# Kernel tuning notes

Hardware: AMD Instinct MI355X
Metric: run time of the kernel (lower is better)

The kernel has to match this reference:

```python
import jax, jax.numpy as jnp
import numpy as np

F_CTX = 16          # ctx_future_context_size
CONV_STRENGTH = 0.5 # ctx_conv_strength
LN_EPS = 1e-5


def _layernorm(x, w, eps=LN_EPS):
    mu = jnp.mean(x, axis=-1, keepdims=True)
    var = jnp.var(x, axis=-1, keepdims=True)
    return (x - mu) / jnp.sqrt(var + eps) * w


def setup_inputs() -> dict:
    key = jax.random.key(0)
    B, S, D, V = 2, 512, 1024, 32000
    k0, k1, k2, k3 = jax.random.split(key, 4)
    emb_norm = jax.random.normal(k0, (B, S, D), jnp.float32)
    W_lm = jax.random.normal(k1, (V, D), jnp.float32) * 0.02
    W_ctx = jax.random.normal(k2, (V, D), jnp.float32) * 0.02
    ln_w = jnp.ones((D,), jnp.float32)
    # labels cover seq_len + F - 1 future tokens (required by the gather/view)
    y = jax.random.randint(k3, (B, S + F_CTX - 1), 0, V, dtype=jnp.int32)
    return {"emb_norm": emb_norm, "W_lm": W_lm, "W_ctx": W_ctx, "ln_w": ln_w, "y": y}


def reference(emb_norm, W_lm, W_ctx, ln_w, y):
    B, S, D = emb_norm.shape
    V = W_lm.shape[0]
    F = F_CTX

    logits = jnp.einsum('bsd,vd->bsv', emb_norm, W_lm)             # lm_head.output_proj
    c = jnp.einsum('bsd,vd->bsv', _layernorm(emb_norm, ln_w), W_ctx)  # context_head

    # y_context[b, s, v] = count of v among the F future tokens y[b, s:s+F]
    # (faithful to gather(indices) + one_hot(...).sum(-2), without the huge one-hot)
    win = jnp.arange(S)[:, None] + jnp.arange(F)[None, :]          # (S, F)
    y_win = y[:, win]                                              # (B, S, F)
    b_idx = jnp.arange(B)[:, None, None]
    s_idx = jnp.arange(S)[None, :, None]
    y_context = jnp.zeros((B, S, V), jnp.float32).at[b_idx, s_idx, y_win].add(1.0)

    # weighted BCE-with-logits (mean over all elements, per-element weight)
    w = 1.0 + 0.5 * jnp.any(y_context > 1.0, axis=0).astype(jnp.float32)   # (S, V)
    t = (y_context > 0.0).astype(jnp.float32)
    bce = jnp.maximum(c, 0.0) - c * t + jnp.log1p(jnp.exp(-jnp.abs(c)))
    context_loss = jnp.mean(w * bce)

    # causal exponential-decay window sum over the last F positions of c
    ed = jnp.exp(-CONV_STRENGTH * jnp.arange(F - 1, -1, -1, dtype=jnp.float32))
    ed = ed / ed.sum()
    c_pad = jnp.pad(c, ((0, 0), (F - 1, 0), (0, 0)))
    context = jnp.zeros_like(c)
    for j in range(F):  # fixed small window (16)
        context = context + ed[j] * c_pad[:, j:j + S, :]

    logits = logits + context

    # cross entropy vs y[:, :-F+1] == y[:, :S], ignore_index = -1
    tgt = y[:, :S]
    logp = jax.nn.log_softmax(logits, axis=-1)
    valid = (tgt >= 0)
    tgt_safe = jnp.where(valid, tgt, 0)
    nll = -jnp.take_along_axis(logp, tgt_safe[..., None].astype(jnp.int32), axis=-1)[..., 0]
    loss = jnp.sum(nll * valid.astype(nll.dtype)) / jnp.maximum(jnp.sum(valid.astype(jnp.float32)), 1.0)

    return logits, loss, context_loss
```

## Files before the change

kernel.cpp:

```cpp
#include <hip/hip_runtime.h>
#include <hip/hip_bf16.h>

typedef unsigned short u16;
typedef unsigned int u32;
typedef __bf16 bf16x8 __attribute__((ext_vector_type(8)));
typedef float f32x4 __attribute__((ext_vector_type(4)));

#define SDIM 512
#define BDIM 2
#define DDIM 1024
#define VDIM 32000
#define FCTX 16
#define NROWS (BDIM * SDIM)
#define YSTR (SDIM + FCTX - 1)
#define CONV_CHUNK 64

__device__ __forceinline__ u16 f2bf(float f) {
    u32 u = __float_as_uint(f);
    u += 0x7fffu + ((u >> 16) & 1u);
    return (u16)(u >> 16);
}

__device__ __forceinline__ void gload_lds16(const void* g, void* l) {
    __builtin_amdgcn_global_load_lds((const __attribute__((address_space(1))) void*)g,
                                     (__attribute__((address_space(3))) void*)l, 16, 0, 0);
}

__global__ __launch_bounds__(256) void prep_a_kernel(
    const float* __restrict__ emb, const float* __restrict__ lnw,
    u16* __restrict__ Alm, u16* __restrict__ Actx)
{
    int row = blockIdx.x;
    int t = threadIdx.x;
    const float4* x4 = (const float4*)(emb + (size_t)row * DDIM);
    float4 v = x4[t];
    float s1 = v.x + v.y + v.z + v.w;
    float s2 = v.x*v.x + v.y*v.y + v.z*v.z + v.w*v.w;
#pragma unroll
    for (int off = 32; off; off >>= 1) {
        s1 += __shfl_down(s1, off, 64);
        s2 += __shfl_down(s2, off, 64);
    }
    __shared__ float r1[4], r2[4];
    int lane = t & 63, wave = t >> 6;
    if (lane == 0) { r1[wave] = s1; r2[wave] = s2; }
    __syncthreads();
    s1 = r1[0] + r1[1] + r1[2] + r1[3];
    s2 = r2[0] + r2[1] + r2[2] + r2[3];
    float mean = s1 * (1.f / DDIM);
    float var = s2 * (1.f / DDIM) - mean * mean;
    float rstd = rsqrtf(var + 1e-5f);
    float4 w = ((const float4*)lnw)[t];
    ushort4 a, b;
    a.x = f2bf(v.x); a.y = f2bf(v.y); a.z = f2bf(v.z); a.w = f2bf(v.w);
    b.x = f2bf((v.x - mean) * rstd * w.x);
    b.y = f2bf((v.y - mean) * rstd * w.y);
    b.z = f2bf((v.z - mean) * rstd * w.z);
    b.w = f2bf((v.w - mean) * rstd * w.w);
    ((ushort4*)(Alm + (size_t)row * DDIM))[t] = a;
    ((ushort4*)(Actx + (size_t)row * DDIM))[t] = b;
}

__global__ __launch_bounds__(256) void cast_kernel(
    const float4* __restrict__ src, ushort4* __restrict__ dst)
{
    int i = blockIdx.x * 256 + threadIdx.x;
    float4 f = src[i];
    ushort4 o;
    o.x = f2bf(f.x); o.y = f2bf(f.y); o.z = f2bf(f.z); o.w = f2bf(f.w);
    dst[i] = o;
}


__device__ __forceinline__ void stage_half(const u16* __restrict__ mat, int grow0, int gcol0,
                                           char* lds_half, int t)
{
    int r0 = t >> 3;
    int swz = ((t & 7) ^ (r0 & 7)) * 8;
    const u16* g0 = mat + (size_t)(grow0 + r0) * DDIM + gcol0 + swz;
    gload_lds16(g0, lds_half + t * 16);
    gload_lds16(g0 + (size_t)64 * DDIM, lds_half + 8192 + t * 16);
}

#define MFMA16(a, b, c) __builtin_amdgcn_mfma_f32_16x16x32_bf16(a, b, c, 0, 0, 0)
#define VM4 asm volatile("s_waitcnt vmcnt(4)" ::: "memory")
#define VM0 asm volatile("s_waitcnt vmcnt(0)" ::: "memory")
#define NOP ((void)0)

#define PHASE(BB, Q, STG, VM) do {                                              \
    bf16x8 a00, a01, a10, a11;                                                  \
    if ((Q) == 0) {                                                             \
        _Pragma("unroll")                                                       \
        for (int j = 0; j < 4; ++j) {                                           \
            bfr[2*j]   = *(const bf16x8*)(Bln + (BB)*65536 + j*2048 + axor0);   \
            bfr[2*j+1] = *(const bf16x8*)(Bln + (BB)*65536 + j*2048 + axor1);   \
        }                                                                       \
    }                                                                           \
    { const char* Ab = Aln + (BB)*65536 + (2*(Q))*2048;                         \
      a00 = *(const bf16x8*)(Ab + axor0);                                       \
      a01 = *(const bf16x8*)(Ab + axor1);                                       \
      a10 = *(const bf16x8*)(Ab + 2048 + axor0);                                \
      a11 = *(const bf16x8*)(Ab + 2048 + axor1); }                              \
    STG; VM;                                                                    \
    __builtin_amdgcn_s_barrier();                                               \
    asm volatile("s_waitcnt lgkmcnt(0)" ::: "memory");                          \
    __builtin_amdgcn_sched_barrier(0);                                          \
    __builtin_amdgcn_s_setprio(1);                                              \
    _Pragma("unroll")                                                           \
    for (int j = 0; j < 4; ++j) {                                               \
        acc[2*(Q)][j]   = MFMA16(a00, bfr[2*j],   acc[2*(Q)][j]);               \
        acc[2*(Q)][j]   = MFMA16(a01, bfr[2*j+1], acc[2*(Q)][j]);               \
        acc[2*(Q)+1][j] = MFMA16(a10, bfr[2*j],   acc[2*(Q)+1][j]);             \
        acc[2*(Q)+1][j] = MFMA16(a11, bfr[2*j+1], acc[2*(Q)+1][j]);             \
    }                                                                           \
    __builtin_amdgcn_s_setprio(0);                                              \
    __builtin_amdgcn_s_barrier();                                               \
} while (0)

#define STAGE_A(BB, H, KT) stage_half(Amat, bm256 + (H)*128, (KT)*64, ldsb + (BB)*65536 + (H)*16384, t)
#define STAGE_B(BB, H, KT) stage_half(Bmat, bn256 + (H)*128, (KT)*64, ldsb + (BB)*65536 + 32768 + (H)*16384, t)

__global__ __launch_bounds__(512, 2) void gemm_kernel(
    const u16* __restrict__ A0, const u16* __restrict__ B0, float* __restrict__ C0,
    const u16* __restrict__ A1, const u16* __restrict__ B1, float* __restrict__ C1)
{
    constexpr int N = VDIM;
    __shared__ __align__(16) char lds_s[131072];
    char* ldsb = lds_s;

    int bid = blockIdx.x;
    int wg = (bid & 7) * 125 + (bid >> 3);
    int z = (wg >= 500) ? 1 : 0;
    int rem = wg - z * 500;
    int bn = rem >> 2, bm = rem & 3;

    const u16* Amat; const u16* Bmat; float* C;
    if (z == 0) { Amat = A0; Bmat = B0; C = C0; }
    else        { Amat = A1; Bmat = B1; C = C1; }

    int t = threadIdx.x;
    int lane = t & 63, wave = t >> 6;
    int wr = wave >> 2, wc = wave & 3;
    int l15 = lane & 15, lg = lane >> 4, l7 = lane & 7;
    int bm256 = bm * 256, bn256 = bn * 256;

    int axor0 = (lg * 16) ^ (l7 << 4);
    int axor1 = (64 + lg * 16) ^ (l7 << 4);
    const char* Aln = ldsb + wr * 16384 + l15 * 128;
    const char* Bln = ldsb + 32768 + (wc >> 1) * 16384 + ((wc & 1) * 64 + l15) * 128;

    f32x4 acc[8][4] = {};
    bf16x8 bfr[8];

    STAGE_A(0, 0, 0); STAGE_A(0, 1, 0); STAGE_B(0, 0, 0); STAGE_B(0, 1, 0);
    STAGE_B(1, 0, 1); STAGE_B(1, 1, 1);
    VM4;
    __builtin_amdgcn_s_barrier();

    for (int m = 0; m < 7; ++m) {
        int k1 = 2 * m + 1, k2 = 2 * m + 2, k3 = 2 * m + 3;
        PHASE(0, 0, STAGE_A(1, 0, k1), NOP);
        PHASE(0, 1, STAGE_A(1, 1, k1), NOP);
        PHASE(0, 2, STAGE_B(0, 0, k2), NOP);
        PHASE(0, 3, STAGE_B(0, 1, k2), VM4);
        PHASE(1, 0, STAGE_A(0, 0, k2), NOP);
        PHASE(1, 1, STAGE_A(0, 1, k2), NOP);
        PHASE(1, 2, STAGE_B(1, 0, k3), NOP);
        PHASE(1, 3, STAGE_B(1, 1, k3), VM4);
    }
    PHASE(0, 0, STAGE_A(1, 0, 15), NOP);
    PHASE(0, 1, STAGE_A(1, 1, 15), NOP);
    PHASE(0, 2, NOP, NOP);
    PHASE(0, 3, NOP, VM0);
    PHASE(1, 0, NOP, NOP);
    PHASE(1, 1, NOP, NOP);
    PHASE(1, 2, NOP, NOP);
    PHASE(1, 3, NOP, NOP);

    int row0 = bm256 + wr * 128 + lg * 4;
    int col0 = bn256 + wc * 64 + l15;
#pragma unroll
    for (int i = 0; i < 8; ++i)
#pragma unroll
        for (int j = 0; j < 4; ++j) {
            float* cp = C + (size_t)(row0 + i * 16) * N + col0 + j * 16;
#pragma unroll
            for (int r = 0; r < 4; ++r) cp[(size_t)r * N] = acc[i][j][r];
        }
}

__global__ __launch_bounds__(256) void conv_kernel(
    const float* __restrict__ c, float* __restrict__ logits, float* __restrict__ acc)
{
    int v = blockIdx.x * 256 + threadIdx.x;
    int s0 = blockIdx.y * CONV_CHUNK;
    int b = blockIdx.z;

    float coef[FCTX];
    float Z = 0.f;
#pragma unroll
    for (int i = 0; i < FCTX; ++i) { coef[i] = expf(-0.5f * i); Z += coef[i]; }
    float invZ = 1.f / Z;
#pragma unroll
    for (int i = 0; i < FCTX; ++i) coef[i] *= invZ;

    float ring[FCTX];
#pragma unroll
    for (int i = 0; i < FCTX; ++i) ring[i] = 0.f;

    size_t base = ((size_t)b * SDIM) * VDIM + v;

    if (s0 > 0) {
#pragma unroll
        for (int i = 1; i < FCTX; ++i) {
            int s = s0 - FCTX + i;
            ring[i] = c[base + (size_t)s * VDIM];
        }
    }

    float sp = 0.f;
    for (int t16 = 0; t16 < CONV_CHUNK; t16 += FCTX) {
#pragma unroll
        for (int u = 0; u < FCTX; ++u) {
            size_t off = base + (size_t)(s0 + t16 + u) * VDIM;
            float cv = c[off];
            ring[u] = cv;
            float ctx = 0.f;
#pragma unroll
            for (int i = 0; i < FCTX; ++i) ctx += coef[i] * ring[(u - i) & (FCTX - 1)];
            logits[off] += ctx;
            sp += fmaxf(cv, 0.f) + log1pf(expf(-fabsf(cv)));
        }
    }
#pragma unroll
    for (int off = 32; off; off >>= 1) sp += __shfl_down(sp, off, 64);
    __shared__ float rs[4];
    int lane = threadIdx.x & 63, wave = threadIdx.x >> 6;
    if (lane == 0) rs[wave] = sp;
    __syncthreads();
    if (threadIdx.x == 0) atomicAdd(acc + 1, rs[0] + rs[1] + rs[2] + rs[3]);
}

__device__ __forceinline__ float softplus(float x) {
    return fmaxf(x, 0.f) + log1pf(expf(-fabsf(x)));
}

__global__ __launch_bounds__(256) void corr_kernel(
    const float* __restrict__ c, const int* __restrict__ y, float* __restrict__ acc)
{
    int sid = blockIdx.x * 256 + threadIdx.x;
    float corr = 0.f;
    if (sid < SDIM) {
        int tok[2 * FCTX];
        for (int i = 0; i < FCTX; ++i) {
            tok[i] = y[sid + i];
            tok[FCTX + i] = y[YSTR + sid + i];
        }
        for (int k = 0; k < 2 * FCTX; ++k) {
            int v = tok[k];
            bool seen = false;
            for (int j = 0; j < k; ++j) seen |= (tok[j] == v);
            if (seen) continue;
            int c0 = 0, c1 = 0;
            for (int i = 0; i < FCTX; ++i) {
                c0 += (tok[i] == v);
                c1 += (tok[FCTX + i] == v);
            }
            float w = ((c0 > 1) || (c1 > 1)) ? 1.5f : 1.0f;
            float cv0 = c[(size_t)sid * VDIM + v];
            float cv1 = c[(size_t)(SDIM + sid) * VDIM + v];
            if (w > 1.f) corr += 0.5f * (softplus(cv0) + softplus(cv1));
            if (c0 > 0) corr -= w * cv0;
            if (c1 > 0) corr -= w * cv1;
        }
    }
    atomicAdd(acc + 1, corr);
}

__global__ __launch_bounds__(256) void loss_kernel(
    const float* __restrict__ logits, const int* __restrict__ y, float* __restrict__ acc)
{
    int row = blockIdx.x;
    int t = threadIdx.x;
    const float* lp = logits + (size_t)row * VDIM;
    float m = -3.4e38f, sum = 0.f;
    for (int i = t; i < VDIM; i += 256) {
        float x = lp[i];
        float nm = fmaxf(m, x);
        sum = sum * expf(m - nm) + expf(x - nm);
        m = nm;
    }
#pragma unroll
    for (int off = 32; off; off >>= 1) {
        float om = __shfl_down(m, off, 64);
        float os = __shfl_down(sum, off, 64);
        float nm = fmaxf(m, om);
        sum = sum * expf(m - nm) + os * expf(om - nm);
        m = nm;
    }
    __shared__ float sm[4], ss[4];
    int lane = t & 63, wave = t >> 6;
    if (lane == 0) { sm[wave] = m; ss[wave] = sum; }
    __syncthreads();
    if (t == 0) {
        float M = sm[0], S = ss[0];
        for (int wv = 1; wv < 4; ++wv) {
            float nm = fmaxf(M, sm[wv]);
            S = S * expf(M - nm) + ss[wv] * expf(sm[wv] - nm);
            M = nm;
        }
        int b = row >> 9, s = row & 511;
        int tgt = y[b * YSTR + s];
        float xt = lp[tgt];
        atomicAdd(acc, -(xt - M - logf(S)));
    }
}

__global__ void finalize_kernel(const float* __restrict__ acc, float* __restrict__ out)
{
    out[(size_t)NROWS * VDIM]     = acc[0] * (1.f / (float)NROWS);
    out[(size_t)NROWS * VDIM + 1] = acc[1] * (1.f / ((float)NROWS * (float)VDIM));
}

extern "C" void kernel_launch(void* const* d_in, const int* in_sizes, int n_in,
                              void* d_out, int out_size, void* d_ws, size_t ws_size,
                              hipStream_t stream)
{
    const float* emb  = (const float*)d_in[0];
    const float* Wlm  = (const float*)d_in[1];
    const float* Wctx = (const float*)d_in[2];
    const float* lnw  = (const float*)d_in[3];
    const int*   y    = (const int*)d_in[4];
    float* out = (float*)d_out;

    char* ws = (char*)d_ws;
    const size_t A_BYTES = (size_t)NROWS * DDIM * 2;
    const size_t W_BYTES = (size_t)VDIM * DDIM * 2;
    const size_t C_BYTES = (size_t)NROWS * VDIM * 4;
    u16*   Alm   = (u16*)ws;
    u16*   Actx  = (u16*)(ws + A_BYTES);
    u16*   WlmB  = (u16*)(ws + 2 * A_BYTES);
    u16*   WctxB = (u16*)(ws + 2 * A_BYTES + W_BYTES);
    float* c     = (float*)(ws + 2 * A_BYTES + 2 * W_BYTES);
    float* acc   = (float*)(ws + 2 * A_BYTES + 2 * W_BYTES + C_BYTES);

    hipMemsetAsync(acc, 0, 2 * sizeof(float), stream);
    prep_a_kernel<<<NROWS, 256, 0, stream>>>(emb, lnw, Alm, Actx);
    cast_kernel<<<(VDIM * DDIM / 4) / 256, 256, 0, stream>>>((const float4*)Wlm,  (ushort4*)WlmB);
    cast_kernel<<<(VDIM * DDIM / 4) / 256, 256, 0, stream>>>((const float4*)Wctx, (ushort4*)WctxB);
    gemm_kernel<<<1000, 512, 0, stream>>>(Alm, WlmB, out, Actx, WctxB, c);
    conv_kernel<<<dim3(VDIM / 256, SDIM / CONV_CHUNK, BDIM), 256, 0, stream>>>(c, out, acc);
    corr_kernel<<<2, 256, 0, stream>>>(c, y, acc);
    loss_kernel<<<NROWS, 256, 0, stream>>>(out, y, acc);
    finalize_kernel<<<1, 1, 0, stream>>>(acc, out);
}
```

Measured before the change: 688.0 us.

## Fold causal context conv into K-concatenated GEMM and drop c materialization

Because the causal decay window is linear, the context term is computed by convolving the normalized activations over sequence and concatenating them with the LM activations along K (K=2048), so one GEMM with a concatenated weight matrix produces logits plus context directly. The context-head GEMM no longer writes c to global memory; it reduces softplus of its accumulators in-register and atomically adds the sum. The BCE target correction recomputes the few needed c values with per-token dot products. This removes the 131MB c write/read and the separate conv pass, at the cost of a longer-K GEMM for half the blocks and extra bf16 rounding of the convolved activations.

```diff
diff --git a/kernel.cpp b/kernel.cpp
--- a/kernel.cpp
+++ b/kernel.cpp
@@ -13,7 +13,7 @@
 #define FCTX 16
 #define NROWS (BDIM * SDIM)
 #define YSTR (SDIM + FCTX - 1)
-#define CONV_CHUNK 64
+#define KCAT 2048
 
 __device__ __forceinline__ u16 f2bf(float f) {
     u32 u = __float_as_uint(f);
@@ -21,6 +21,14 @@
     return (u16)(u >> 16);
 }
 
+__device__ __forceinline__ float bf2f(u16 u) {
+    return __uint_as_float((u32)u << 16);
+}
+
+__device__ __forceinline__ float softplus(float x) {
+    return fmaxf(x, 0.f) + log1pf(expf(-fabsf(x)));
+}
+
 __device__ __forceinline__ void gload_lds16(const void* g, void* l) {
     __builtin_amdgcn_global_load_lds((const __attribute__((address_space(1))) void*)g,
                                      (__attribute__((address_space(3))) void*)l, 16, 0, 0);
@@ -28,7 +36,7 @@
 
 __global__ __launch_bounds__(256) void prep_a_kernel(
     const float* __restrict__ emb, const float* __restrict__ lnw,
-    u16* __restrict__ Alm, u16* __restrict__ Actx)
+    u16* __restrict__ Acat, u16* __restrict__ ActxB)
 {
     int row = blockIdx.x;
     int t = threadIdx.x;
@@ -57,29 +65,59 @@
     b.y = f2bf((v.y - mean) * rstd * w.y);
     b.z = f2bf((v.z - mean) * rstd * w.z);
     b.w = f2bf((v.w - mean) * rstd * w.w);
-    ((ushort4*)(Alm + (size_t)row * DDIM))[t] = a;
-    ((ushort4*)(Actx + (size_t)row * DDIM))[t] = b;
+    ((ushort4*)(Acat + (size_t)row * KCAT))[t] = a;
+    ((ushort4*)(ActxB + (size_t)row * DDIM))[t] = b;
+}
+
+__global__ __launch_bounds__(256) void prep_conv_kernel(
+    const u16* __restrict__ ActxB, u16* __restrict__ Acat)
+{
+    int row = blockIdx.x;
+    int s = row & (SDIM - 1);
+    int t = threadIdx.x;
+    float coef[FCTX];
+    float Z = 0.f;
+#pragma unroll
+    for (int i = 0; i < FCTX; ++i) { coef[i] = expf(-0.5f * i); Z += coef[i]; }
+    float invZ = 1.f / Z;
+    float4 sum = {0.f, 0.f, 0.f, 0.f};
+#pragma unroll
+    for (int i = 0; i < FCTX; ++i) {
+        if (s - i >= 0) {
+            ushort4 q = *(const ushort4*)(ActxB + (size_t)(row - i) * DDIM + t * 4);
+            float k = coef[i] * invZ;
+            sum.x += k * bf2f(q.x);
+            sum.y += k * bf2f(q.y);
+            sum.z += k * bf2f(q.z);
+            sum.w += k * bf2f(q.w);
+        }
+    }
+    ushort4 o;
+    o.x = f2bf(sum.x); o.y = f2bf(sum.y); o.z = f2bf(sum.z); o.w = f2bf(sum.w);
+    *(ushort4*)(Acat + (size_t)row * KCAT + DDIM + t * 4) = o;
 }
 
 __global__ __launch_bounds__(256) void cast_kernel(
-    const float4* __restrict__ src, ushort4* __restrict__ dst)
+    const float4* __restrict__ src, u16* __restrict__ dstBase, int colOff)
 {
     int i = blockIdx.x * 256 + threadIdx.x;
+    int v = i >> 8;
+    int d4 = i & 255;
     float4 f = src[i];
     ushort4 o;
     o.x = f2bf(f.x); o.y = f2bf(f.y); o.z = f2bf(f.z); o.w = f2bf(f.w);
-    dst[i] = o;
-}
-
-
-__device__ __forceinline__ void stage_half(const u16* __restrict__ mat, int grow0, int gcol0,
-                                           char* lds_half, int t)
+    *(ushort4*)(dstBase + (size_t)v * KCAT + colOff + d4 * 4) = o;
+}
+
+
+__device__ __forceinline__ void stage_half(const u16* __restrict__ mat, int lda,
+                                           int grow0, int gcol0, char* lds_half, int t)
 {
     int r0 = t >> 3;
     int swz = ((t & 7) ^ (r0 & 7)) * 8;
-    const u16* g0 = mat + (size_t)(grow0 + r0) * DDIM + gcol0 + swz;
+    const u16* g0 = mat + (size_t)(grow0 + r0) * lda + gcol0 + swz;
     gload_lds16(g0, lds_half + t * 16);
-    gload_lds16(g0 + (size_t)64 * DDIM, lds_half + 8192 + t * 16);
+    gload_lds16(g0 + (size_t)64 * lda, lds_half + 8192 + t * 16);
 }
 
 #define MFMA16(a, b, c) __builtin_amdgcn_mfma_f32_16x16x32_bf16(a, b, c, 0, 0, 0)
@@ -117,28 +155,17 @@
     __builtin_amdgcn_s_barrier();                                               \
 } while (0)
 
-#define STAGE_A(BB, H, KT) stage_half(Amat, bm256 + (H)*128, (KT)*64, ldsb + (BB)*65536 + (H)*16384, t)
-#define STAGE_B(BB, H, KT) stage_half(Bmat, bn256 + (H)*128, (KT)*64, ldsb + (BB)*65536 + 32768 + (H)*16384, t)
-
-__global__ __launch_bounds__(512, 2) void gemm_kernel(
-    const u16* __restrict__ A0, const u16* __restrict__ B0, float* __restrict__ C0,
-    const u16* __restrict__ A1, const u16* __restrict__ B1, float* __restrict__ C1)
+#define STAGE_A(BB, H, KT) stage_half(Amat, LDA, bm256 + (H)*128, (KT)*64, ldsb + (BB)*65536 + (H)*16384, t)
+#define STAGE_B(BB, H, KT) stage_half(Bmat, LDB, bn256 + (H)*128, (KT)*64, ldsb + (BB)*65536 + 32768 + (H)*16384, t)
+
+template<int KD, int LDA, int LDB, bool SP>
+__device__ __forceinline__ void gemm_core(
+    const u16* __restrict__ Amat, const u16* __restrict__ Bmat,
+    float* __restrict__ C, float* __restrict__ accbuf,
+    char* ldsb, int bm, int bn, int t)
 {
     constexpr int N = VDIM;
-    __shared__ __align__(16) char lds_s[131072];
-    char* ldsb = lds_s;
-
-    int bid = blockIdx.x;
-    int wg = (bid & 7) * 125 + (bid >> 3);
-    int z = (wg >= 500) ? 1 : 0;
-    int rem = wg - z * 500;
-    int bn = rem >> 2, bm = rem & 3;
-
-    const u16* Amat; const u16* Bmat; float* C;
-    if (z == 0) { Amat = A0; Bmat = B0; C = C0; }
-    else        { Amat = A1; Bmat = B1; C = C1; }
-
-    int t = threadIdx.x;
+    constexpr int NKT = KD / 64;
     int lane = t & 63, wave = t >> 6;
     int wr = wave >> 2, wc = wave & 3;
     int l15 = lane & 15, lg = lane >> 4, l7 = lane & 7;
@@ -157,7 +184,7 @@
     VM4;
     __builtin_amdgcn_s_barrier();
 
-    for (int m = 0; m < 7; ++m) {
+    for (int m = 0; m < NKT / 2 - 1; ++m) {
         int k1 = 2 * m + 1, k2 = 2 * m + 2, k3 = 2 * m + 3;
         PHASE(0, 0, STAGE_A(1, 0, k1), NOP);
         PHASE(0, 1, STAGE_A(1, 1, k1), NOP);
@@ -168,8 +195,8 @@
         PHASE(1, 2, STAGE_B(1, 0, k3), NOP);
         PHASE(1, 3, STAGE_B(1, 1, k3), VM4);
     }
-    PHASE(0, 0, STAGE_A(1, 0, 15), NOP);
-    PHASE(0, 1, STAGE_A(1, 1, 15), NOP);
+    PHASE(0, 0, STAGE_A(1, 0, NKT - 1), NOP);
+    PHASE(0, 1, STAGE_A(1, 1, NKT - 1), NOP);
     PHASE(0, 2, NOP, NOP);
     PHASE(0, 3, NOP, VM0);
     PHASE(1, 0, NOP, NOP);
@@ -177,104 +204,104 @@
     PHASE(1, 2, NOP, NOP);
     PHASE(1, 3, NOP, NOP);
 
-    int row0 = bm256 + wr * 128 + lg * 4;
-    int col0 = bn256 + wc * 64 + l15;
-#pragma unroll
-    for (int i = 0; i < 8; ++i)
-#pragma unroll
-        for (int j = 0; j < 4; ++j) {
-            float* cp = C + (size_t)(row0 + i * 16) * N + col0 + j * 16;
-#pragma unroll
-            for (int r = 0; r < 4; ++r) cp[(size_t)r * N] = acc[i][j][r];
-        }
-}
-
-__global__ __launch_bounds__(256) void conv_kernel(
-    const float* __restrict__ c, float* __restrict__ logits, float* __restrict__ acc)
-{
-    int v = blockIdx.x * 256 + threadIdx.x;
-    int s0 = blockIdx.y * CONV_CHUNK;
-    int b = blockIdx.z;
-
-    float coef[FCTX];
-    float Z = 0.f;
-#pragma unroll
-    for (int i = 0; i < FCTX; ++i) { coef[i] = expf(-0.5f * i); Z += coef[i]; }
-    float invZ = 1.f / Z;
-#pragma unroll
-    for (int i = 0; i < FCTX; ++i) coef[i] *= invZ;
-
-    float ring[FCTX];
-#pragma unroll
-    for (int i = 0; i < FCTX; ++i) ring[i] = 0.f;
-
-    size_t base = ((size_t)b * SDIM) * VDIM + v;
-
-    if (s0 > 0) {
-#pragma unroll
-        for (int i = 1; i < FCTX; ++i) {
-            int s = s0 - FCTX + i;
-            ring[i] = c[base + (size_t)s * VDIM];
-        }
-    }
-
-    float sp = 0.f;
-    for (int t16 = 0; t16 < CONV_CHUNK; t16 += FCTX) {
-#pragma unroll
-        for (int u = 0; u < FCTX; ++u) {
-            size_t off = base + (size_t)(s0 + t16 + u) * VDIM;
-            float cv = c[off];
-            ring[u] = cv;
-            float ctx = 0.f;
-#pragma unroll
-            for (int i = 0; i < FCTX; ++i) ctx += coef[i] * ring[(u - i) & (FCTX - 1)];
-            logits[off] += ctx;
-            sp += fmaxf(cv, 0.f) + log1pf(expf(-fabsf(cv)));
-        }
-    }
-#pragma unroll
-    for (int off = 32; off; off >>= 1) sp += __shfl_down(sp, off, 64);
+    if constexpr (!SP) {
+        int row0 = bm256 + wr * 128 + lg * 4;
+        int col0 = bn256 + wc * 64 + l15;
+#pragma unroll
+        for (int i = 0; i < 8; ++i)
+#pragma unroll
+            for (int j = 0; j < 4; ++j) {
+                float* cp = C + (size_t)(row0 + i * 16) * N + col0 + j * 16;
+#pragma unroll
+                for (int r = 0; r < 4; ++r) cp[(size_t)r * N] = acc[i][j][r];
+            }
+    } else {
+        float sp = 0.f;
+#pragma unroll
+        for (int i = 0; i < 8; ++i)
+#pragma unroll
+            for (int j = 0; j < 4; ++j)
+#pragma unroll
+                for (int r = 0; r < 4; ++r)
+                    sp += softplus(acc[i][j][r]);
+#pragma unroll
+        for (int off = 32; off; off >>= 1) sp += __shfl_down(sp, off, 64);
+        __syncthreads();
+        float* red = (float*)ldsb;
+        if (lane == 0) red[wave] = sp;
+        __syncthreads();
+        if (t == 0) {
+            float s = 0.f;
+            for (int w2 = 0; w2 < 8; ++w2) s += red[w2];
+            atomicAdd(accbuf + 1, s);
+        }
+    }
+}
+
+__global__ __launch_bounds__(512, 2) void gemm_kernel(
+    const u16* __restrict__ Acat, const u16* __restrict__ Wcat, float* __restrict__ out,
+    const u16* __restrict__ ActxB, float* __restrict__ accbuf)
+{
+    __shared__ __align__(16) char lds_s[131072];
+    int bid = blockIdx.x;
+    int wg = (bid & 7) * 125 + (bid >> 3);
+    int z = (wg >= 500) ? 1 : 0;
+    int rem = wg - z * 500;
+    int bn = rem >> 2, bm = rem & 3;
+    if (z == 0)
+        gemm_core<KCAT, KCAT, KCAT, false>(Acat, Wcat, out, nullptr, lds_s, bm, bn, threadIdx.x);
+    else
+        gemm_core<DDIM, DDIM, KCAT, true>(ActxB, Wcat + DDIM, nullptr, accbuf, lds_s, bm, bn, threadIdx.x);
+}
+
+__global__ __launch_bounds__(256) void corr_kernel(
+    const u16* __restrict__ ActxB, const u16* __restrict__ Wcat,
+    const int* __restrict__ y, float* __restrict__ acc)
+{
+    int gid = blockIdx.x * 256 + threadIdx.x;
+    int sid = gid >> 5, k = gid & 31;
+    int tok[2 * FCTX];
+#pragma unroll
+    for (int i = 0; i < FCTX; ++i) {
+        tok[i] = y[sid + i];
+        tok[FCTX + i] = y[YSTR + sid + i];
+    }
+    float corr = 0.f;
+    int v = tok[k];
+    bool seen = false;
+#pragma unroll
+    for (int j = 0; j < 2 * FCTX; ++j) seen |= ((j < k) && (tok[j] == v));
+    if (!seen) {
+        int c0 = 0, c1 = 0;
+#pragma unroll
+        for (int i = 0; i < FCTX; ++i) {
+            c0 += (tok[i] == v);
+            c1 += (tok[FCTX + i] == v);
+        }
+        float w = ((c0 > 1) || (c1 > 1)) ? 1.5f : 1.0f;
+        const u16* a0 = ActxB + (size_t)sid * DDIM;
+        const u16* a1 = ActxB + (size_t)(SDIM + sid) * DDIM;
+        const u16* wv = Wcat + (size_t)v * KCAT + DDIM;
+        float cv0 = 0.f, cv1 = 0.f;
+        for (int d = 0; d < DDIM; d += 4) {
+            ushort4 wq = *(const ushort4*)(wv + d);
+            ushort4 q0 = *(const ushort4*)(a0 + d);
+            ushort4 q1 = *(const ushort4*)(a1 + d);
+            float w0 = bf2f(wq.x), w1 = bf2f(wq.y), w2 = bf2f(wq.z), w3 = bf2f(wq.w);
+            cv0 += bf2f(q0.x) * w0 + bf2f(q0.y) * w1 + bf2f(q0.z) * w2 + bf2f(q0.w) * w3;
+            cv1 += bf2f(q1.x) * w0 + bf2f(q1.y) * w1 + bf2f(q1.z) * w2 + bf2f(q1.w) * w3;
+        }
+        if (w > 1.f) corr += 0.5f * (softplus(cv0) + softplus(cv1));
+        if (c0 > 0) corr -= w * cv0;
+        if (c1 > 0) corr -= w * cv1;
+    }
+#pragma unroll
+    for (int off = 32; off; off >>= 1) corr += __shfl_down(corr, off, 64);
     __shared__ float rs[4];
     int lane = threadIdx.x & 63, wave = threadIdx.x >> 6;
-    if (lane == 0) rs[wave] = sp;
+    if (lane == 0) rs[wave] = corr;
     __syncthreads();
     if (threadIdx.x == 0) atomicAdd(acc + 1, rs[0] + rs[1] + rs[2] + rs[3]);
-}
-
-__device__ __forceinline__ float softplus(float x) {
-    return fmaxf(x, 0.f) + log1pf(expf(-fabsf(x)));
-}
-
-__global__ __launch_bounds__(256) void corr_kernel(
-    const float* __restrict__ c, const int* __restrict__ y, float* __restrict__ acc)
-{
-    int sid = blockIdx.x * 256 + threadIdx.x;
-    float corr = 0.f;
-    if (sid < SDIM) {
-        int tok[2 * FCTX];
-        for (int i = 0; i < FCTX; ++i) {
-            tok[i] = y[sid + i];
-            tok[FCTX + i] = y[YSTR + sid + i];
-        }
-        for (int k = 0; k < 2 * FCTX; ++k) {
-            int v = tok[k];
-            bool seen = false;
-            for (int j = 0; j < k; ++j) seen |= (tok[j] == v);
-            if (seen) continue;
-            int c0 = 0, c1 = 0;
-            for (int i = 0; i < FCTX; ++i) {
-                c0 += (tok[i] == v);
-                c1 += (tok[FCTX + i] == v);
-            }
-            float w = ((c0 > 1) || (c1 > 1)) ? 1.5f : 1.0f;
-            float cv0 = c[(size_t)sid * VDIM + v];
-            float cv1 = c[(size_t)(SDIM + sid) * VDIM + v];
-            if (w > 1.f) corr += 0.5f * (softplus(cv0) + softplus(cv1));
-            if (c0 > 0) corr -= w * cv0;
-            if (c1 > 0) corr -= w * cv1;
-        }
-    }
-    atomicAdd(acc + 1, corr);
 }
 
 __global__ __launch_bounds__(256) void loss_kernel(
@@ -334,23 +361,21 @@
     float* out = (float*)d_out;
 
     char* ws = (char*)d_ws;
-    const size_t A_BYTES = (size_t)NROWS * DDIM * 2;
-    const size_t W_BYTES = (size_t)VDIM * DDIM * 2;
-    const size_t C_BYTES = (size_t)NROWS * VDIM * 4;
-    u16*   Alm   = (u16*)ws;
-    u16*   Actx  = (u16*)(ws + A_BYTES);
-    u16*   WlmB  = (u16*)(ws + 2 * A_BYTES);
-    u16*   WctxB = (u16*)(ws + 2 * A_BYTES + W_BYTES);
-    float* c     = (float*)(ws + 2 * A_BYTES + 2 * W_BYTES);
-    float* acc   = (float*)(ws + 2 * A_BYTES + 2 * W_BYTES + C_BYTES);
+    const size_t ACAT_BYTES = (size_t)NROWS * KCAT * 2;
+    const size_t ACTX_BYTES = (size_t)NROWS * DDIM * 2;
+    const size_t WCAT_BYTES = (size_t)VDIM * KCAT * 2;
+    u16*   Acat  = (u16*)ws;
+    u16*   ActxB = (u16*)(ws + ACAT_BYTES);
+    u16*   Wcat  = (u16*)(ws + ACAT_BYTES + ACTX_BYTES);
+    float* acc   = (float*)(ws + ACAT_BYTES + ACTX_BYTES + WCAT_BYTES);
 
     hipMemsetAsync(acc, 0, 2 * sizeof(float), stream);
-    prep_a_kernel<<<NROWS, 256, 0, stream>>>(emb, lnw, Alm, Actx);
-    cast_kernel<<<(VDIM * DDIM / 4) / 256, 256, 0, stream>>>((const float4*)Wlm,  (ushort4*)WlmB);
-    cast_kernel<<<(VDIM * DDIM / 4) / 256, 256, 0, stream>>>((const float4*)Wctx, (ushort4*)WctxB);
-    gemm_kernel<<<1000, 512, 0, stream>>>(Alm, WlmB, out, Actx, WctxB, c);
-    conv_kernel<<<dim3(VDIM / 256, SDIM / CONV_CHUNK, BDIM), 256, 0, stream>>>(c, out, acc);
-    corr_kernel<<<2, 256, 0, stream>>>(c, y, acc);
+    prep_a_kernel<<<NROWS, 256, 0, stream>>>(emb, lnw, Acat, ActxB);
+    prep_conv_kernel<<<NROWS, 256, 0, stream>>>(ActxB, Acat);
+    cast_kernel<<<(VDIM * DDIM / 4) / 256, 256, 0, stream>>>((const float4*)Wlm,  Wcat, 0);
+    cast_kernel<<<(VDIM * DDIM / 4) / 256, 256, 0, stream>>>((const float4*)Wctx, Wcat, DDIM);
+    gemm_kernel<<<1000, 512, 0, stream>>>(Acat, Wcat, out, ActxB, acc);
+    corr_kernel<<<64, 256, 0, stream>>>(ActxB, Wcat, y, acc);
     loss_kernel<<<NROWS, 256, 0, stream>>>(out, y, acc);
     finalize_kernel<<<1, 1, 0, stream>>>(acc, out);
 }
```

Result: no change. 680.2 us (-1.1%).
